# Performance work log

Measured on AMD Instinct MI355X. Metric: run time of the kernel, lower is better.

Reference implementation:

```python
import jax, jax.numpy as jnp
import numpy as np

VOCAB_SIZE = 256
CODEC_VOCAB = 1024  # 2 ** codec_bits
D = 1024
NHEAD = 16
FF = 4096
L = 6
ENROLLED = 225  # enrolled_codec_sec(3) * codec_rate(75)
B, TT, TA = 4, 128, 512


def sinusoidal_pe(T, d):
    pos = np.arange(T, dtype=np.float32)[:, None]
    div = np.exp(np.arange(0, d, 2, dtype=np.float32) * (-np.log(10000.0) / d))
    pe = np.zeros((T, d), dtype=np.float32)
    pe[:, 0::2] = np.sin(pos * div)
    pe[:, 1::2] = np.cos(pos * div)
    return jnp.asarray(pe)


def layernorm(x, w, b, eps=1e-5):
    mu = x.mean(-1, keepdims=True)
    var = ((x - mu) ** 2).mean(-1, keepdims=True)
    return (x - mu) * jax.lax.rsqrt(var + eps) * w + b


def mha(q_in, kv_in, in_w, in_b, out_w, out_b, mask=None):
    # q_in: [B,Tq,D], kv_in: [B,Tk,D]; mask True == blocked (torch attn_mask convention)
    d = q_in.shape[-1]
    h, hd = NHEAD, d // NHEAD
    wq, wk, wv = in_w[:d], in_w[d:2 * d], in_w[2 * d:]
    bq, bk, bv = in_b[:d], in_b[d:2 * d], in_b[2 * d:]
    Bq, Tq, _ = q_in.shape
    Tk = kv_in.shape[1]
    q = (q_in @ wq.T + bq).reshape(Bq, Tq, h, hd)
    k = (kv_in @ wk.T + bk).reshape(Bq, Tk, h, hd)
    v = (kv_in @ wv.T + bv).reshape(Bq, Tk, h, hd)
    scores = jnp.einsum('bqhd,bkhd->bhqk', q, k) / jnp.sqrt(jnp.float32(hd))
    if mask is not None:
        scores = jnp.where(mask, -jnp.inf, scores)
    attn = jax.nn.softmax(scores, axis=-1)
    o = jnp.einsum('bhqk,bkhd->bqhd', attn, v).reshape(Bq, Tq, d)
    return o @ out_w.T + out_b


def pack(te, ae, ee, tl, al):
    # Ragged concat [text[:tl]; audio[:al]; enrolled] padded to static max_len.
    Tt, Ta, Te = te.shape[0], ae.shape[0], ee.shape[0]
    pos = jnp.arange(Tt + Ta + Te)
    t = te[jnp.clip(pos, 0, Tt - 1)]
    a = ae[jnp.clip(pos - tl, 0, Ta - 1)]
    e = ee[jnp.clip(pos - tl - al, 0, Te - 1)]
    x = jnp.where((pos < tl)[:, None], t,
        jnp.where((pos < tl + al)[:, None], a,
        jnp.where((pos < tl + al + Te)[:, None], e, jnp.zeros_like(t))))
    return x


def setup_inputs():
    key = jax.random.key(0)
    ks = iter(jax.random.split(key, 64))

    def n(shape, s=0.02):
        return jax.random.normal(next(ks), shape, dtype=jnp.float32) * s

    text = jax.random.randint(next(ks), (B, TT), 0, VOCAB_SIZE)
    audio = jax.random.randint(next(ks), (B, TA), 0, CODEC_VOCAB)
    enrolled_audio = jax.random.randint(next(ks), (B, ENROLLED), 0, CODEC_VOCAB)
    # force sample 0 to full length so max_len is static (= TT+TA+ENROLLED)
    text_len_batch = jax.random.randint(next(ks), (B,), TT // 2, TT + 1).at[0].set(TT)
    audio_len_batch = jax.random.randint(next(ks), (B,), TA // 2, TA + 1).at[0].set(TA)
    return dict(
        text=text, audio=audio, enrolled_audio=enrolled_audio,
        text_len_batch=text_len_batch, audio_len_batch=audio_len_batch,
        text_emb=n((VOCAB_SIZE, D)), audio_emb=n((CODEC_VOCAB, D)),
        sa_in_w=n((L, 3 * D, D)), sa_in_b=jnp.zeros((L, 3 * D), jnp.float32),
        sa_out_w=n((L, D, D)), sa_out_b=jnp.zeros((L, D), jnp.float32),
        ca_in_w=n((L, 3 * D, D)), ca_in_b=jnp.zeros((L, 3 * D), jnp.float32),
        ca_out_w=n((L, D, D)), ca_out_b=jnp.zeros((L, D), jnp.float32),
        ff1_w=n((L, FF, D)), ff1_b=jnp.zeros((L, FF), jnp.float32),
        ff2_w=n((L, D, FF)), ff2_b=jnp.zeros((L, D), jnp.float32),
        ln1_w=jnp.ones((L, D), jnp.float32), ln1_b=jnp.zeros((L, D), jnp.float32),
        ln2_w=jnp.ones((L, D), jnp.float32), ln2_b=jnp.zeros((L, D), jnp.float32),
        ln3_w=jnp.ones((L, D), jnp.float32), ln3_b=jnp.zeros((L, D), jnp.float32),
        out_w=n((CODEC_VOCAB, D)), out_b=jnp.zeros((CODEC_VOCAB,), jnp.float32))


def reference(text, audio, enrolled_audio, text_len_batch, audio_len_batch,
              text_emb, audio_emb, sa_in_w, sa_in_b, sa_out_w, sa_out_b,
              ca_in_w, ca_in_b, ca_out_w, ca_out_b, ff1_w, ff1_b, ff2_w, ff2_b,
              ln1_w, ln1_b, ln2_w, ln2_b, ln3_w, ln3_b, out_w, out_b):
    # per-segment sinusoidal PE (positions reset at the start of each segment)
    te = text_emb[text] + sinusoidal_pe(text.shape[1], D)
    ae = audio_emb[audio] + sinusoidal_pe(audio.shape[1], D)
    ee = audio_emb[enrolled_audio] + sinusoidal_pe(enrolled_audio.shape[1], D)
    embed = jax.vmap(pack)(te, ae, ee, text_len_batch, audio_len_batch)  # [B, max_len, D]
    max_len = embed.shape[1]
    prefix = text.shape[1] + audio.shape[1]  # == max(tl+al) by construction
    mask = jnp.triu(jnp.ones((max_len, max_len), bool), 1).at[:, :prefix].set(False)
    mem = embed  # TransformerDecoder memory == embed
    x = embed
    for l in range(L):  # post-norm decoder layers (torch default norm_first=False)
        x = layernorm(x + mha(x, x, sa_in_w[l], sa_in_b[l], sa_out_w[l], sa_out_b[l], mask), ln1_w[l], ln1_b[l])
        x = layernorm(x + mha(x, mem, ca_in_w[l], ca_in_b[l], ca_out_w[l], ca_out_b[l]), ln2_w[l], ln2_b[l])
        h = jax.nn.relu(x @ ff1_w[l].T + ff1_b[l]) @ ff2_w[l].T + ff2_b[l]
        x = layernorm(x + h, ln3_w[l], ln3_b[l])
    return x @ out_w.T + out_b  # [B, max_len, CODEC_VOCAB]
```

## Files before the change

### kernel.cpp

```cpp
#include <hip/hip_runtime.h>
#include <hip/hip_bf16.h>

#define B_      4
#define TT_     128
#define TA_     512
#define TE_     225
#define T_      865
#define D_      1024
#define H_      16
#define FF_     4096
#define L_      6
#define PREFIX_ 640
#define M_TOK   (B_ * T_)
#define M_PAD   3584

typedef __attribute__((ext_vector_type(8))) short          s16x8;
typedef __attribute__((ext_vector_type(4))) float          f32x4;
typedef __attribute__((ext_vector_type(8))) unsigned short u16x8;

typedef __attribute__((address_space(1))) const void gv_t;
typedef __attribute__((address_space(3))) void       lv_t;

__device__ __forceinline__ float bf2f(unsigned short u) {
  union { unsigned int i; float f; } c; c.i = ((unsigned int)u) << 16; return c.f;
}
__device__ __forceinline__ unsigned short f2bf(float f) {
  union { __hip_bfloat16 h; unsigned short u; } c; c.h = __float2bfloat16(f); return c.u;
}

__global__ __launch_bounds__(256) void embed_kernel(
    const int* __restrict__ text, const int* __restrict__ audio,
    const int* __restrict__ enrolled, const int* __restrict__ tl_b,
    const int* __restrict__ al_b, const float* __restrict__ text_emb,
    const float* __restrict__ audio_emb,
    float* __restrict__ xf, unsigned short* __restrict__ xb,
    unsigned short* __restrict__ memb, unsigned short* __restrict__ attnb) {
  int row = blockIdx.x;
  int d0 = threadIdx.x * 4;
  size_t off = (size_t)row * D_ + d0;
  if (row >= M_TOK) {
    *(unsigned long long*)&xb[off]    = 0ull;
    *(unsigned long long*)&memb[off]  = 0ull;
    *(unsigned long long*)&attnb[off] = 0ull;
    return;
  }
  int b = row / T_, pos = row - b * T_;
  int tl = tl_b[b], al = al_b[b];
  const float* emb = nullptr;
  int p = 0;
  if (pos < tl) {
    emb = text_emb + (size_t)text[b * TT_ + pos] * D_;
    p = pos;
  } else if (pos < tl + al) {
    emb = audio_emb + (size_t)audio[b * TA_ + (pos - tl)] * D_;
    p = pos - tl;
  } else if (pos < tl + al + TE_) {
    emb = audio_emb + (size_t)enrolled[b * TE_ + (pos - tl - al)] * D_;
    p = pos - tl - al;
  }
  float4 v;
  float* pv = (float*)&v;
  if (emb) {
    const float c = -9.2103403719761836f / (float)D_;
    #pragma unroll
    for (int e = 0; e < 4; ++e) {
      int d = d0 + e;
      int i = d >> 1;
      float freq = expf(c * (float)(2 * i));
      float arg = (float)p * freq;
      float pe = (d & 1) ? cosf(arg) : sinf(arg);
      pv[e] = emb[d] + pe;
    }
  } else {
    v = make_float4(0.f, 0.f, 0.f, 0.f);
  }
  *(float4*)&xf[off] = v;
  unsigned long long pk = (unsigned long long)f2bf(pv[0])
      | ((unsigned long long)f2bf(pv[1]) << 16)
      | ((unsigned long long)f2bf(pv[2]) << 32)
      | ((unsigned long long)f2bf(pv[3]) << 48);
  *(unsigned long long*)&xb[off]   = pk;
  *(unsigned long long*)&memb[off] = pk;
}

__global__ __launch_bounds__(256) void cvt_kernel(
    const float* __restrict__ in, unsigned short* __restrict__ out, int n8) {
  int i = blockIdx.x * 256 + threadIdx.x;
  if (i >= n8) return;
  const float4* pp = (const float4*)in + (size_t)i * 2;
  float4 a = pp[0], bq = pp[1];
  u16x8 o;
  o[0] = f2bf(a.x);  o[1] = f2bf(a.y);  o[2] = f2bf(a.z);  o[3] = f2bf(a.w);
  o[4] = f2bf(bq.x); o[5] = f2bf(bq.y); o[6] = f2bf(bq.z); o[7] = f2bf(bq.w);
  *(u16x8*)(out + (size_t)i * 8) = o;
}

__global__ __launch_bounds__(256) void cvt_layer_kernel(
    const float* __restrict__ s0, const float* __restrict__ s1,
    const float* __restrict__ s2, const float* __restrict__ s3,
    const float* __restrict__ s4, const float* __restrict__ s5,
    unsigned short* __restrict__ dst) {
  size_t e = ((size_t)blockIdx.x * 256 + threadIdx.x) * 8;
  if (e >= 16777216u) return;
  const float* src; size_t off;
  if      (e <  3145728u) { src = s0; off = e; }
  else if (e <  4194304u) { src = s1; off = e -  3145728u; }
  else if (e <  7340032u) { src = s2; off = e -  4194304u; }
  else if (e <  8388608u) { src = s3; off = e -  7340032u; }
  else if (e < 12582912u) { src = s4; off = e -  8388608u; }
  else                    { src = s5; off = e - 12582912u; }
  const float4* pp = (const float4*)(src + off);
  float4 a = pp[0], bq = pp[1];
  u16x8 o;
  o[0] = f2bf(a.x);  o[1] = f2bf(a.y);  o[2] = f2bf(a.z);  o[3] = f2bf(a.w);
  o[4] = f2bf(bq.x); o[5] = f2bf(bq.y); o[6] = f2bf(bq.z); o[7] = f2bf(bq.w);
  *(u16x8*)(dst + e) = o;
}

template <int BM, int BN, int ACT, int OBF>
__global__ __launch_bounds__(256) void gemm_bf16(
    const unsigned short* __restrict__ A, int lda,
    const unsigned short* __restrict__ W, int ldw,
    const float* __restrict__ bias,
    float* __restrict__ Cf, unsigned short* __restrict__ Cb, int ldc,
    int Mw, int K) {
  constexpr int WROWS = BM / 2, WCOLS = BN / 2;
  constexpr int WM = WROWS / 16, WN = WCOLS / 16;
  constexpr int ACH = BM / 64, BCH = BN / 64;
  __shared__ unsigned short lgA[2][BM * 32];
  __shared__ unsigned short lgB[2][BN * 32];
  int tid = threadIdx.x, lane = tid & 63, wid = tid >> 6;

  int gx = gridDim.x;
  int nwg = gx * gridDim.y;
  int orig = blockIdx.y * gx + blockIdx.x;
  int q = nwg >> 3, r = nwg & 7;
  int xcd = orig & 7, loc = orig >> 3;
  int wg = (xcd < r ? xcd * (q + 1) : r * (q + 1) + (xcd - r) * q) + loc;
  int m0 = (wg / gx) * BM, n0 = (wg % gx) * BN;

  int wr = wid >> 1, wc = wid & 1;
  int lrow = lane >> 2, lk = (lane & 3) * 8;

  const unsigned short* gAp[ACH];
  const unsigned short* gBp[BCH];
  unsigned aoff[ACH], boff[BCH];
  #pragma unroll
  for (int c = 0; c < ACH; ++c) {
    int row0 = wid * (16 * ACH) + 16 * c;
    gAp[c] = A + (size_t)(m0 + row0 + lrow) * lda + lk;
    aoff[c] = row0 * 32;
  }
  #pragma unroll
  for (int c = 0; c < BCH; ++c) {
    int row0 = wid * (16 * BCH) + 16 * c;
    gBp[c] = W + (size_t)(n0 + row0 + lrow) * ldw + lk;
    boff[c] = row0 * 32;
  }

  f32x4 acc[WM][WN];
  #pragma unroll
  for (int i = 0; i < WM; ++i)
    #pragma unroll
    for (int j = 0; j < WN; ++j) acc[i][j] = (f32x4)0.f;

  int frow = lane & 15, fk = (lane >> 4) * 8;

  #pragma unroll
  for (int c = 0; c < ACH; ++c)
    __builtin_amdgcn_global_load_lds((gv_t*)gAp[c], (lv_t*)&lgA[0][aoff[c]], 16, 0, 0);
  #pragma unroll
  for (int c = 0; c < BCH; ++c)
    __builtin_amdgcn_global_load_lds((gv_t*)gBp[c], (lv_t*)&lgB[0][boff[c]], 16, 0, 0);
  __syncthreads();

  int nt = K / 32;
  for (int t = 0; t < nt; ++t) {
    int cur = t & 1;
    if (t + 1 < nt) {
      int k0 = (t + 1) * 32;
      #pragma unroll
      for (int c = 0; c < ACH; ++c)
        __builtin_amdgcn_global_load_lds((gv_t*)(gAp[c] + k0),
                                         (lv_t*)&lgA[cur ^ 1][aoff[c]], 16, 0, 0);
      #pragma unroll
      for (int c = 0; c < BCH; ++c)
        __builtin_amdgcn_global_load_lds((gv_t*)(gBp[c] + k0),
                                         (lv_t*)&lgB[cur ^ 1][boff[c]], 16, 0, 0);
    }
    s16x8 af[WM], bfr[WN];
    #pragma unroll
    for (int i = 0; i < WM; ++i)
      af[i] = *(const s16x8*)&lgA[cur][(wr * WROWS + i * 16 + frow) * 32 + fk];
    #pragma unroll
    for (int j = 0; j < WN; ++j)
      bfr[j] = *(const s16x8*)&lgB[cur][(wc * WCOLS + j * 16 + frow) * 32 + fk];
    __builtin_amdgcn_s_setprio(1);
    #pragma unroll
    for (int i = 0; i < WM; ++i)
      #pragma unroll
      for (int j = 0; j < WN; ++j)
        acc[i][j] = __builtin_amdgcn_mfma_f32_16x16x32_bf16(af[i], bfr[j], acc[i][j], 0, 0, 0);
    __builtin_amdgcn_s_setprio(0);
    __syncthreads();
  }

  float bv[WN];
  #pragma unroll
  for (int j = 0; j < WN; ++j) bv[j] = bias[n0 + wc * WCOLS + j * 16 + (lane & 15)];
  int rbase = m0 + wr * WROWS + (lane >> 4) * 4;
  int cbase = n0 + wc * WCOLS + (lane & 15);
  #pragma unroll
  for (int i = 0; i < WM; ++i)
    #pragma unroll
    for (int rr = 0; rr < 4; ++rr) {
      int m = rbase + i * 16 + rr;
      if (m < Mw) {
        #pragma unroll
        for (int j = 0; j < WN; ++j) {
          float v = acc[i][j][rr] + bv[j];
          if (ACT) v = fmaxf(v, 0.f);
          if (OBF) Cb[(size_t)m * ldc + cbase + j * 16] = f2bf(v);
          else     Cf[(size_t)m * ldc + cbase + j * 16] = v;
        }
      }
    }
}

template <bool MASKED>
__global__ __launch_bounds__(256) void attn_mfma(
    const unsigned short* __restrict__ qkv,
    unsigned short* __restrict__ out) {
  __shared__ unsigned short KsL[64 * 64];
  __shared__ unsigned short VtL[64 * 72];
  __shared__ unsigned short PsL[4][16 * 64];
  int tid = threadIdx.x;
  int lane = tid & 63, wid = tid >> 6;
  int b = blockIdx.y >> 4, h = blockIdx.y & 15;
  int q0 = blockIdx.x * 64;
  int r16 = lane & 15, g4 = lane >> 4;

  int qrow = q0 + wid * 16 + r16;
  if (qrow >= T_) qrow = T_ - 1;
  const unsigned short* qbase =
      qkv + (size_t)(b * T_ + qrow) * 3072 + h * 64 + g4 * 8;
  s16x8 qf0 = *(const s16x8*)qbase;
  s16x8 qf1 = *(const s16x8*)(qbase + 32);

  float m_[4], l_[4];
  f32x4 o_[4];
  #pragma unroll
  for (int rg = 0; rg < 4; ++rg) { m_[rg] = -INFINITY; l_[rg] = 0.f; }
  #pragma unroll
  for (int dj = 0; dj < 4; ++dj) o_[dj] = (f32x4)0.f;

  const int nt = MASKED ? max(10, (int)blockIdx.x + 1) : 14;

  for (int t = 0; t < nt; ++t) {
    int k0 = t * 64;
    __syncthreads();

    #pragma unroll
    for (int c = 0; c < 2; ++c) {
      int row = wid * 16 + c * 8 + (lane >> 3);
      int kr = k0 + row; if (kr >= T_) kr = T_ - 1;
      int grp = (lane & 7) ^ (row & 7);
      const unsigned short* src =
          qkv + (size_t)(b * T_ + kr) * 3072 + 1024 + h * 64 + grp * 8;
      __builtin_amdgcn_global_load_lds((gv_t*)src,
          (lv_t*)&KsL[(wid * 16 + c * 8) * 64], 16, 0, 0);
    }
    {
      int vkr = k0 + lane; if (vkr >= T_) vkr = T_ - 1;
      const unsigned short* vsrc =
          qkv + (size_t)(b * T_ + vkr) * 3072 + 2048 + h * 64 + wid * 16;
      u16x8 v0 = *(const u16x8*)vsrc;
      u16x8 v1 = *(const u16x8*)(vsrc + 8);
      #pragma unroll
      for (int jj = 0; jj < 8; ++jj) {
        VtL[(wid * 16 + jj) * 72 + lane]     = v0[jj];
        VtL[(wid * 16 + 8 + jj) * 72 + lane] = v1[jj];
      }
    }
    __syncthreads();

    f32x4 sj[4];
    #pragma unroll
    for (int j = 0; j < 4; ++j) sj[j] = (f32x4)0.f;
    __builtin_amdgcn_s_setprio(1);
    #pragma unroll
    for (int j = 0; j < 4; ++j) {
      int krow = j * 16 + r16;
      s16x8 kf0 = *(const s16x8*)&KsL[krow * 64 + ((g4 ^ (krow & 7)) * 8)];
      s16x8 kf1 = *(const s16x8*)&KsL[krow * 64 + (((4 + g4) ^ (krow & 7)) * 8)];
      sj[j] = __builtin_amdgcn_mfma_f32_16x16x32_bf16(qf0, kf0, sj[j], 0, 0, 0);
      sj[j] = __builtin_amdgcn_mfma_f32_16x16x32_bf16(qf1, kf1, sj[j], 0, 0, 0);
    }
    __builtin_amdgcn_s_setprio(0);

    float alpha_[4];
    #pragma unroll
    for (int rg = 0; rg < 4; ++rg) {
      int qa = q0 + wid * 16 + g4 * 4 + rg;
      float pm = -INFINITY;
      #pragma unroll
      for (int j = 0; j < 4; ++j) {
        int kg = k0 + j * 16 + r16;
        float sv = sj[j][rg] * 0.125f;
        bool bad = (kg >= T_) || (MASKED && kg > qa && kg >= PREFIX_);
        sv = bad ? -INFINITY : sv;
        sj[j][rg] = sv;
        pm = fmaxf(pm, sv);
      }
      pm = fmaxf(pm, __shfl_xor(pm, 1));
      pm = fmaxf(pm, __shfl_xor(pm, 2));
      pm = fmaxf(pm, __shfl_xor(pm, 4));
      pm = fmaxf(pm, __shfl_xor(pm, 8));
      float mn = fmaxf(m_[rg], pm);
      float al = __expf(m_[rg] - mn);
      m_[rg] = mn;
      alpha_[rg] = al;
      int prow = g4 * 4 + rg;
      float ps = 0.f;
      #pragma unroll
      for (int j = 0; j < 4; ++j) {
        float pv = __expf(sj[j][rg] - mn);
        ps += pv;
        PsL[wid][prow * 64 + (((j * 2 + (r16 >> 3)) ^ (prow & 7)) * 8) + (r16 & 7)]
            = f2bf(pv);
      }
      ps += __shfl_xor(ps, 1);
      ps += __shfl_xor(ps, 2);
      ps += __shfl_xor(ps, 4);
      ps += __shfl_xor(ps, 8);
      l_[rg] = l_[rg] * al + ps;
    }
    #pragma unroll
    for (int dj = 0; dj < 4; ++dj)
      #pragma unroll
      for (int rg = 0; rg < 4; ++rg) o_[dj][rg] *= alpha_[rg];

    __builtin_amdgcn_s_setprio(1);
    #pragma unroll
    for (int kk = 0; kk < 2; ++kk) {
      s16x8 pf = *(const s16x8*)
          &PsL[wid][r16 * 64 + (((kk * 4 + g4) ^ (r16 & 7)) * 8)];
      #pragma unroll
      for (int dj = 0; dj < 4; ++dj) {
        s16x8 vf = *(const s16x8*)
            &VtL[(dj * 16 + r16) * 72 + kk * 32 + g4 * 8];
        o_[dj] = __builtin_amdgcn_mfma_f32_16x16x32_bf16(pf, vf, o_[dj], 0, 0, 0);
      }
    }
    __builtin_amdgcn_s_setprio(0);
  }

  #pragma unroll
  for (int rg = 0; rg < 4; ++rg) {
    int qa = q0 + wid * 16 + g4 * 4 + rg;
    if (qa < T_) {
      float inv = 1.f / l_[rg];
      unsigned short* ob = out + (size_t)(b * T_ + qa) * D_ + h * 64;
      #pragma unroll
      for (int dj = 0; dj < 4; ++dj)
        ob[dj * 16 + r16] = f2bf(o_[dj][rg] * inv);
    }
  }
}

__global__ __launch_bounds__(256) void ln_res_kernel(
    float* __restrict__ x, const float* __restrict__ r,
    const float* __restrict__ w, const float* __restrict__ b,
    unsigned short* __restrict__ xb) {
  __shared__ float red[4];
  int row = blockIdx.x, tid = threadIdx.x;
  size_t off = (size_t)row * D_ + tid * 4;
  float4 xv = *(float4*)&x[off];
  float4 rv = *(const float4*)&r[off];
  float v0 = xv.x + rv.x, v1 = xv.y + rv.y, v2 = xv.z + rv.z, v3 = xv.w + rv.w;

  float s = v0 + v1 + v2 + v3;
  #pragma unroll
  for (int o = 1; o < 64; o <<= 1) s += __shfl_xor(s, o);
  if ((tid & 63) == 0) red[tid >> 6] = s;
  __syncthreads();
  float mu = (red[0] + red[1] + red[2] + red[3]) * (1.f / 1024.f);
  __syncthreads();

  float d0 = v0 - mu, d1 = v1 - mu, d2 = v2 - mu, d3 = v3 - mu;
  float ss = d0 * d0 + d1 * d1 + d2 * d2 + d3 * d3;
  #pragma unroll
  for (int o = 1; o < 64; o <<= 1) ss += __shfl_xor(ss, o);
  if ((tid & 63) == 0) red[tid >> 6] = ss;
  __syncthreads();
  float var = (red[0] + red[1] + red[2] + red[3]) * (1.f / 1024.f);
  float rs = rsqrtf(var + 1e-5f);

  float4 wv = *(const float4*)&w[tid * 4];
  float4 bv = *(const float4*)&b[tid * 4];
  float o0 = d0 * rs * wv.x + bv.x, o1 = d1 * rs * wv.y + bv.y;
  float o2 = d2 * rs * wv.z + bv.z, o3 = d3 * rs * wv.w + bv.w;
  *(float4*)&x[off] = make_float4(o0, o1, o2, o3);
  unsigned long long pk = (unsigned long long)f2bf(o0)
      | ((unsigned long long)f2bf(o1) << 16)
      | ((unsigned long long)f2bf(o2) << 32)
      | ((unsigned long long)f2bf(o3) << 48);
  *(unsigned long long*)&xb[off] = pk;
}

extern "C" void kernel_launch(void* const* d_in, const int* in_sizes, int n_in,
                              void* d_out, int out_size, void* d_ws, size_t ws_size,
                              hipStream_t stream) {
  const int* text       = (const int*)d_in[0];
  const int* audio      = (const int*)d_in[1];
  const int* enrolled   = (const int*)d_in[2];
  const int* tl_b       = (const int*)d_in[3];
  const int* al_b       = (const int*)d_in[4];
  const float* text_emb = (const float*)d_in[5];
  const float* audio_emb= (const float*)d_in[6];
  const float* sa_in_w  = (const float*)d_in[7];
  const float* sa_in_b  = (const float*)d_in[8];
  const float* sa_out_w = (const float*)d_in[9];
  const float* sa_out_b = (const float*)d_in[10];
  const float* ca_in_w  = (const float*)d_in[11];
  const float* ca_in_b  = (const float*)d_in[12];
  const float* ca_out_w = (const float*)d_in[13];
  const float* ca_out_b = (const float*)d_in[14];
  const float* ff1_w    = (const float*)d_in[15];
  const float* ff1_b    = (const float*)d_in[16];
  const float* ff2_w    = (const float*)d_in[17];
  const float* ff2_b    = (const float*)d_in[18];
  const float* ln1_w    = (const float*)d_in[19];
  const float* ln1_b    = (const float*)d_in[20];
  const float* ln2_w    = (const float*)d_in[21];
  const float* ln2_b    = (const float*)d_in[22];
  const float* ln3_w    = (const float*)d_in[23];
  const float* ln3_b    = (const float*)d_in[24];
  const float* out_w    = (const float*)d_in[25];
  const float* out_b    = (const float*)d_in[26];

  char* p = (char*)d_ws;
  float* xf = (float*)p;            p += (size_t)M_PAD * D_ * 4;
  float* tmp = (float*)p;           p += (size_t)M_PAD * D_ * 4;
  unsigned short* xb = (unsigned short*)p;    p += (size_t)M_PAD * D_ * 2;
  unsigned short* memb = (unsigned short*)p;  p += (size_t)M_PAD * D_ * 2;
  unsigned short* qkv = (unsigned short*)p;   p += (size_t)M_PAD * FF_ * 2;
  unsigned short* attnb = (unsigned short*)p; p += (size_t)M_PAD * D_ * 2;
  unsigned short* wbuf = (unsigned short*)p;  p += (size_t)16777216 * 2;
  unsigned short* outwb = (unsigned short*)p; p += (size_t)1048576 * 2;

  unsigned short* w_sa_qkv = wbuf;
  unsigned short* w_sa_o   = wbuf + 3145728;
  unsigned short* w_ca_qkv = wbuf + 4194304;
  unsigned short* w_ca_o   = wbuf + 7340032;
  unsigned short* w_ff1    = wbuf + 8388608;
  unsigned short* w_ff2    = wbuf + 12582912;

  embed_kernel<<<M_PAD, 256, 0, stream>>>(text, audio, enrolled, tl_b, al_b,
                                          text_emb, audio_emb, xf, xb, memb, attnb);
  cvt_kernel<<<512, 256, 0, stream>>>(out_w, outwb, 131072);

  for (int l = 0; l < L_; ++l) {
    const float* sa_in_w_l  = sa_in_w  + (size_t)l * 3 * D_ * D_;
    const float* sa_in_b_l  = sa_in_b  + (size_t)l * 3 * D_;
    const float* sa_out_w_l = sa_out_w + (size_t)l * D_ * D_;
    const float* sa_out_b_l = sa_out_b + (size_t)l * D_;
    const float* ca_in_w_l  = ca_in_w  + (size_t)l * 3 * D_ * D_;
    const float* ca_in_b_l  = ca_in_b  + (size_t)l * 3 * D_;
    const float* ca_out_w_l = ca_out_w + (size_t)l * D_ * D_;
    const float* ca_out_b_l = ca_out_b + (size_t)l * D_;
    const float* ff1_w_l    = ff1_w    + (size_t)l * FF_ * D_;
    const float* ff1_b_l    = ff1_b    + (size_t)l * FF_;
    const float* ff2_w_l    = ff2_w    + (size_t)l * D_ * FF_;
    const float* ff2_b_l    = ff2_b    + (size_t)l * D_;

    cvt_layer_kernel<<<8192, 256, 0, stream>>>(sa_in_w_l, sa_out_w_l, ca_in_w_l,
                                               ca_out_w_l, ff1_w_l, ff2_w_l, wbuf);

    gemm_bf16<128, 128, 0, 1><<<dim3(3 * D_ / 128, M_PAD / 128), 256, 0, stream>>>(
        xb, D_, w_sa_qkv, D_, sa_in_b_l, nullptr, qkv, 3 * D_, M_PAD, D_);
    attn_mfma<true><<<dim3(14, B_ * H_), 256, 0, stream>>>(qkv, attnb);
    gemm_bf16<64, 64, 0, 0><<<dim3(D_ / 64, M_PAD / 64), 256, 0, stream>>>(
        attnb, D_, w_sa_o, D_, sa_out_b_l, tmp, nullptr, D_, M_PAD, D_);
    ln_res_kernel<<<M_TOK, 256, 0, stream>>>(xf, tmp, ln1_w + l * D_, ln1_b + l * D_, xb);

    gemm_bf16<64, 64, 0, 1><<<dim3(D_ / 64, M_PAD / 64), 256, 0, stream>>>(
        xb, D_, w_ca_qkv, D_, ca_in_b_l, nullptr, qkv, 3 * D_, M_PAD, D_);
    gemm_bf16<64, 64, 0, 1><<<dim3(2 * D_ / 64, M_PAD / 64), 256, 0, stream>>>(
        memb, D_, w_ca_qkv + (size_t)D_ * D_, D_, ca_in_b_l + D_,
        nullptr, qkv + D_, 3 * D_, M_PAD, D_);
    attn_mfma<false><<<dim3(14, B_ * H_), 256, 0, stream>>>(qkv, attnb);
    gemm_bf16<64, 64, 0, 0><<<dim3(D_ / 64, M_PAD / 64), 256, 0, stream>>>(
        attnb, D_, w_ca_o, D_, ca_out_b_l, tmp, nullptr, D_, M_PAD, D_);
    ln_res_kernel<<<M_TOK, 256, 0, stream>>>(xf, tmp, ln2_w + l * D_, ln2_b + l * D_, xb);

    gemm_bf16<128, 128, 1, 1><<<dim3(FF_ / 128, M_PAD / 128), 256, 0, stream>>>(
        xb, D_, w_ff1, D_, ff1_b_l, nullptr, qkv, FF_, M_PAD, D_);
    gemm_bf16<64, 64, 0, 0><<<dim3(D_ / 64, M_PAD / 64), 256, 0, stream>>>(
        qkv, FF_, w_ff2, FF_, ff2_b_l, tmp, nullptr, D_, M_PAD, FF_);
    ln_res_kernel<<<M_TOK, 256, 0, stream>>>(xf, tmp, ln3_w + l * D_, ln3_b + l * D_, xb);
  }

  gemm_bf16<64, 64, 0, 0><<<dim3(D_ / 64, M_PAD / 64), 256, 0, stream>>>(
      xb, D_, outwb, D_, out_b, (float*)d_out, nullptr, D_, M_TOK, D_);
}
```

Before: 2.288 ms.

## Triple-buffer GEMM with swizzled LDS and batch cross-attention KV projections across layers

Replaces the double-buffered GEMM with a three-stage pipeline. It uses explicit vmcnt waits, a single barrier per iteration, an XOR-swizzled LDS layout to avoid bank conflicts, and BK=64 for the 64x64 tiles. Because cross-attention K/V depend only on the fixed memory, the K/V weights for all six layers are converted once and projected in one large GEMM up front. This removes six smaller per-layer GEMMs and gives better tile utilization. The cost is a large extra workspace buffer, with a fallback path used when the workspace is too small.

New measurement: 2.216 ms. 3.1% less time.

```diff
diff --git a/kernel.cpp b/kernel.cpp
--- a/kernel.cpp
+++ b/kernel.cpp
@@ -13,6 +13,7 @@
 #define PREFIX_ 640
 #define M_TOK   (B_ * T_)
 #define M_PAD   3584
+#define NKV     (L_ * 2 * D_)
 
 typedef __attribute__((ext_vector_type(8))) short          s16x8;
 typedef __attribute__((ext_vector_type(4))) float          f32x4;
@@ -26,6 +27,9 @@
 }
 __device__ __forceinline__ unsigned short f2bf(float f) {
   union { __hip_bfloat16 h; unsigned short u; } c; c.h = __float2bfloat16(f); return c.u;
+}
+template <int N> __device__ __forceinline__ void vmwait() {
+  asm volatile("s_waitcnt vmcnt(%0)" :: "n"(N) : "memory");
 }
 
 __global__ __launch_bounds__(256) void embed_kernel(
@@ -117,8 +121,31 @@
   *(u16x8*)(dst + e) = o;
 }
 
-template <int BM, int BN, int ACT, int OBF>
-__global__ __launch_bounds__(256) void gemm_bf16(
+__global__ __launch_bounds__(256) void cvt_ckv_w(
+    const float* __restrict__ ca_in_w, unsigned short* __restrict__ wckv) {
+  int rr = blockIdx.x;
+  int l = rr / (2 * D_), w = rr % (2 * D_);
+  const float* src = ca_in_w + (size_t)l * 3 * D_ * D_ + (size_t)(D_ + w) * D_;
+  unsigned short* dst = wckv + (size_t)rr * D_;
+  int c = threadIdx.x * 4;
+  float4 v4 = *(const float4*)(src + c);
+  unsigned long long pk = (unsigned long long)f2bf(v4.x)
+      | ((unsigned long long)f2bf(v4.y) << 16)
+      | ((unsigned long long)f2bf(v4.z) << 32)
+      | ((unsigned long long)f2bf(v4.w) << 48);
+  *(unsigned long long*)&dst[c] = pk;
+}
+
+__global__ __launch_bounds__(256) void cvt_ckv_b(
+    const float* __restrict__ ca_in_b, float* __restrict__ cbias) {
+  int rr = blockIdx.x * 256 + threadIdx.x;
+  if (rr >= NKV) return;
+  int l = rr / (2 * D_), w = rr % (2 * D_);
+  cbias[rr] = ca_in_b[(size_t)l * 3 * D_ + D_ + w];
+}
+
+template <int BM, int BN, int BK, int ACT, int OBF>
+__global__ __launch_bounds__(256) void gemm_p2(
     const unsigned short* __restrict__ A, int lda,
     const unsigned short* __restrict__ W, int ldw,
     const float* __restrict__ bias,
@@ -126,11 +153,16 @@
     int Mw, int K) {
   constexpr int WROWS = BM / 2, WCOLS = BN / 2;
   constexpr int WM = WROWS / 16, WN = WCOLS / 16;
-  constexpr int ACH = BM / 64, BCH = BN / 64;
-  __shared__ unsigned short lgA[2][BM * 32];
-  __shared__ unsigned short lgB[2][BN * 32];
+  constexpr int LPR = BK / 8;
+  constexpr int RPI = 64 / LPR;
+  constexpr int ACH = (BM / 4) / RPI;
+  constexpr int BCH = (BN / 4) / RPI;
+  constexpr int ABUF = BM * BK, BBUF = BN * BK;
+  constexpr int KSUB = BK / 32;
+  constexpr int LW = ACH + BCH;
+  __shared__ unsigned short lds[3 * (ABUF + BBUF)];
+
   int tid = threadIdx.x, lane = tid & 63, wid = tid >> 6;
-
   int gx = gridDim.x;
   int nwg = gx * gridDim.y;
   int orig = blockIdx.y * gx + blockIdx.x;
@@ -140,22 +172,23 @@
   int m0 = (wg / gx) * BM, n0 = (wg % gx) * BN;
 
   int wr = wid >> 1, wc = wid & 1;
-  int lrow = lane >> 2, lk = (lane & 3) * 8;
-
-  const unsigned short* gAp[ACH];
-  const unsigned short* gBp[BCH];
-  unsigned aoff[ACH], boff[BCH];
+  int lrow = lane / LPR, lgrp = lane % LPR;
+  int skey = (BK == 32) ? ((lrow >> 1) & 3) : (lrow & 7);
+  int lk = (lgrp ^ skey) * 8;
+
+  const unsigned short* gAp[ACH]; unsigned aoff[ACH];
+  const unsigned short* gBp[BCH]; unsigned boff[BCH];
   #pragma unroll
   for (int c = 0; c < ACH; ++c) {
-    int row0 = wid * (16 * ACH) + 16 * c;
+    int row0 = wid * (BM / 4) + c * RPI;
     gAp[c] = A + (size_t)(m0 + row0 + lrow) * lda + lk;
-    aoff[c] = row0 * 32;
+    aoff[c] = row0 * BK;
   }
   #pragma unroll
   for (int c = 0; c < BCH; ++c) {
-    int row0 = wid * (16 * BCH) + 16 * c;
+    int row0 = wid * (BN / 4) + c * RPI;
     gBp[c] = W + (size_t)(n0 + row0 + lrow) * ldw + lk;
-    boff[c] = row0 * 32;
+    boff[c] = row0 * BK;
   }
 
   f32x4 acc[WM][WN];
@@ -164,45 +197,53 @@
     #pragma unroll
     for (int j = 0; j < WN; ++j) acc[i][j] = (f32x4)0.f;
 
-  int frow = lane & 15, fk = (lane >> 4) * 8;
-
-  #pragma unroll
-  for (int c = 0; c < ACH; ++c)
-    __builtin_amdgcn_global_load_lds((gv_t*)gAp[c], (lv_t*)&lgA[0][aoff[c]], 16, 0, 0);
-  #pragma unroll
-  for (int c = 0; c < BCH; ++c)
-    __builtin_amdgcn_global_load_lds((gv_t*)gBp[c], (lv_t*)&lgB[0][boff[c]], 16, 0, 0);
-  __syncthreads();
-
-  int nt = K / 32;
+  int frow = lane & 15, g4 = lane >> 4;
+
+  auto STAGE = [&](int bi, int t) {
+    int k0 = t * BK;
+    #pragma unroll
+    for (int c = 0; c < ACH; ++c)
+      __builtin_amdgcn_global_load_lds((gv_t*)(gAp[c] + k0),
+          (lv_t*)&lds[bi * ABUF + aoff[c]], 16, 0, 0);
+    #pragma unroll
+    for (int c = 0; c < BCH; ++c)
+      __builtin_amdgcn_global_load_lds((gv_t*)(gBp[c] + k0),
+          (lv_t*)&lds[3 * ABUF + bi * BBUF + boff[c]], 16, 0, 0);
+  };
+
+  STAGE(0, 0);
+  STAGE(1, 1);
+  int nt = K / BK;
+  int cur = 0;
   for (int t = 0; t < nt; ++t) {
-    int cur = t & 1;
-    if (t + 1 < nt) {
-      int k0 = (t + 1) * 32;
-      #pragma unroll
-      for (int c = 0; c < ACH; ++c)
-        __builtin_amdgcn_global_load_lds((gv_t*)(gAp[c] + k0),
-                                         (lv_t*)&lgA[cur ^ 1][aoff[c]], 16, 0, 0);
-      #pragma unroll
-      for (int c = 0; c < BCH; ++c)
-        __builtin_amdgcn_global_load_lds((gv_t*)(gBp[c] + k0),
-                                         (lv_t*)&lgB[cur ^ 1][boff[c]], 16, 0, 0);
-    }
-    s16x8 af[WM], bfr[WN];
-    #pragma unroll
-    for (int i = 0; i < WM; ++i)
-      af[i] = *(const s16x8*)&lgA[cur][(wr * WROWS + i * 16 + frow) * 32 + fk];
-    #pragma unroll
-    for (int j = 0; j < WN; ++j)
-      bfr[j] = *(const s16x8*)&lgB[cur][(wc * WCOLS + j * 16 + frow) * 32 + fk];
-    __builtin_amdgcn_s_setprio(1);
-    #pragma unroll
-    for (int i = 0; i < WM; ++i)
+    if (t + 1 < nt) vmwait<LW>(); else vmwait<0>();
+    __builtin_amdgcn_s_barrier();
+    if (t + 2 < nt) {
+      int stb = cur + 2; if (stb >= 3) stb -= 3;
+      STAGE(stb, t + 2);
+    }
+    const unsigned short* Ab = &lds[cur * ABUF];
+    const unsigned short* Bb = &lds[3 * ABUF + cur * BBUF];
+    #pragma unroll
+    for (int kk = 0; kk < KSUB; ++kk) {
+      int rk = (BK == 32) ? ((g4 ^ ((frow >> 1) & 3)) * 8)
+                          : (((kk * 4 + g4) ^ (frow & 7)) * 8);
+      s16x8 af[WM], bfr[WN];
+      #pragma unroll
+      for (int i = 0; i < WM; ++i)
+        af[i] = *(const s16x8*)&Ab[(wr * WROWS + i * 16 + frow) * BK + rk];
       #pragma unroll
       for (int j = 0; j < WN; ++j)
-        acc[i][j] = __builtin_amdgcn_mfma_f32_16x16x32_bf16(af[i], bfr[j], acc[i][j], 0, 0, 0);
-    __builtin_amdgcn_s_setprio(0);
-    __syncthreads();
+        bfr[j] = *(const s16x8*)&Bb[(wc * WCOLS + j * 16 + frow) * BK + rk];
+      __builtin_amdgcn_s_setprio(1);
+      #pragma unroll
+      for (int i = 0; i < WM; ++i)
+        #pragma unroll
+        for (int j = 0; j < WN; ++j)
+          acc[i][j] = __builtin_amdgcn_mfma_f32_16x16x32_bf16(af[i], bfr[j], acc[i][j], 0, 0, 0);
+      __builtin_amdgcn_s_setprio(0);
+    }
+    cur = (cur == 2) ? 0 : cur + 1;
   }
 
   float bv[WN];
@@ -229,7 +270,9 @@
 
 template <bool MASKED>
 __global__ __launch_bounds__(256) void attn_mfma(
-    const unsigned short* __restrict__ qkv,
+    const unsigned short* __restrict__ qp, int qld,
+    const unsigned short* __restrict__ kp,
+    const unsigned short* __restrict__ vp, int kvld,
     unsigned short* __restrict__ out) {
   __shared__ unsigned short KsL[64 * 64];
   __shared__ unsigned short VtL[64 * 72];
@@ -243,7 +286,7 @@
   int qrow = q0 + wid * 16 + r16;
   if (qrow >= T_) qrow = T_ - 1;
   const unsigned short* qbase =
-      qkv + (size_t)(b * T_ + qrow) * 3072 + h * 64 + g4 * 8;
+      qp + (size_t)(b * T_ + qrow) * qld + h * 64 + g4 * 8;
   s16x8 qf0 = *(const s16x8*)qbase;
   s16x8 qf1 = *(const s16x8*)(qbase + 32);
 
@@ -266,14 +309,14 @@
       int kr = k0 + row; if (kr >= T_) kr = T_ - 1;
       int grp = (lane & 7) ^ (row & 7);
       const unsigned short* src =
-          qkv + (size_t)(b * T_ + kr) * 3072 + 1024 + h * 64 + grp * 8;
+          kp + (size_t)(b * T_ + kr) * kvld + h * 64 + grp * 8;
       __builtin_amdgcn_global_load_lds((gv_t*)src,
           (lv_t*)&KsL[(wid * 16 + c * 8) * 64], 16, 0, 0);
     }
     {
       int vkr = k0 + lane; if (vkr >= T_) vkr = T_ - 1;
       const unsigned short* vsrc =
-          qkv + (size_t)(b * T_ + vkr) * 3072 + 2048 + h * 64 + wid * 16;
+          vp + (size_t)(b * T_ + vkr) * kvld + h * 64 + wid * 16;
       u16x8 v0 = *(const u16x8*)vsrc;
       u16x8 v1 = *(const u16x8*)(vsrc + 8);
       #pragma unroll
@@ -448,6 +491,10 @@
   unsigned short* attnb = (unsigned short*)p; p += (size_t)M_PAD * D_ * 2;
   unsigned short* wbuf = (unsigned short*)p;  p += (size_t)16777216 * 2;
   unsigned short* outwb = (unsigned short*)p; p += (size_t)1048576 * 2;
+  unsigned short* ckv  = (unsigned short*)p;  p += (size_t)M_PAD * NKV * 2;
+  unsigned short* wckv = (unsigned short*)p;  p += (size_t)NKV * D_ * 2;
+  float* cbias = (float*)p;                   p += (size_t)NKV * 4;
+  bool fused = ((size_t)(p - (char*)d_ws)) <= ws_size;
 
   unsigned short* w_sa_qkv = wbuf;
   unsigned short* w_sa_o   = wbuf + 3145728;
@@ -459,6 +506,13 @@
   embed_kernel<<<M_PAD, 256, 0, stream>>>(text, audio, enrolled, tl_b, al_b,
                                           text_emb, audio_emb, xf, xb, memb, attnb);
   cvt_kernel<<<512, 256, 0, stream>>>(out_w, outwb, 131072);
+
+  if (fused) {
+    cvt_ckv_w<<<NKV, 256, 0, stream>>>(ca_in_w, wckv);
+    cvt_ckv_b<<<NKV / 256, 256, 0, stream>>>(ca_in_b, cbias);
+    gemm_p2<128, 128, 32, 0, 1><<<dim3(NKV / 128, M_PAD / 128), 256, 0, stream>>>(
+        memb, D_, wckv, D_, cbias, nullptr, ckv, NKV, M_PAD, D_);
+  }
 
   for (int l = 0; l < L_; ++l) {
     const float* sa_in_w_l  = sa_in_w  + (size_t)l * 3 * D_ * D_;
@@ -477,30 +531,38 @@
     cvt_layer_kernel<<<8192, 256, 0, stream>>>(sa_in_w_l, sa_out_w_l, ca_in_w_l,
                                                ca_out_w_l, ff1_w_l, ff2_w_l, wbuf);
 
-    gemm_bf16<128, 128, 0, 1><<<dim3(3 * D_ / 128, M_PAD / 128), 256, 0, stream>>>(
+    gemm_p2<128, 128, 32, 0, 1><<<dim3(3 * D_ / 128, M_PAD / 128), 256, 0, stream>>>(
         xb, D_, w_sa_qkv, D_, sa_in_b_l, nullptr, qkv, 3 * D_, M_PAD, D_);
-    attn_mfma<true><<<dim3(14, B_ * H_), 256, 0, stream>>>(qkv, attnb);
-    gemm_bf16<64, 64, 0, 0><<<dim3(D_ / 64, M_PAD / 64), 256, 0, stream>>>(
+    attn_mfma<true><<<dim3(14, B_ * H_), 256, 0, stream>>>(
+        qkv, 3 * D_, qkv + D_, qkv + 2 * D_, 3 * D_, attnb);
+    gemm_p2<64, 64, 64, 0, 0><<<dim3(D_ / 64, M_PAD / 64), 256, 0, stream>>>(
         attnb, D_, w_sa_o, D_, sa_out_b_l, tmp, nullptr, D_, M_PAD, D_);
     ln_res_kernel<<<M_TOK, 256, 0, stream>>>(xf, tmp, ln1_w + l * D_, ln1_b + l * D_, xb);
 
-    gemm_bf16<64, 64, 0, 1><<<dim3(D_ / 64, M_PAD / 64), 256, 0, stream>>>(
+    gemm_p2<64, 64, 64, 0, 1><<<dim3(D_ / 64, M_PAD / 64), 256, 0, stream>>>(
         xb, D_, w_ca_qkv, D_, ca_in_b_l, nullptr, qkv, 3 * D_, M_PAD, D_);
-    gemm_bf16<64, 64, 0, 1><<<dim3(2 * D_ / 64, M_PAD / 64), 256, 0, stream>>>(
-        memb, D_, w_ca_qkv + (size_t)D_ * D_, D_, ca_in_b_l + D_,
-        nullptr, qkv + D_, 3 * D_, M_PAD, D_);
-    attn_mfma<false><<<dim3(14, B_ * H_), 256, 0, stream>>>(qkv, attnb);
-    gemm_bf16<64, 64, 0, 0><<<dim3(D_ / 64, M_PAD / 64), 256, 0, stream>>>(
+    if (fused) {
+      attn_mfma<false><<<dim3(14, B_ * H_), 256, 0, stream>>>(
+          qkv, 3 * D_, ckv + (size_t)l * 2 * D_, ckv + (size_t)l * 2 * D_ + D_,
+          NKV, attnb);
+    } else {
+      gemm_p2<64, 64, 64, 0, 1><<<dim3(2 * D_ / 64, M_PAD / 64), 256, 0, stream>>>(
+          memb, D_, w_ca_qkv + (size_t)D_ * D_, D_, ca_in_b_l + D_,
+          nullptr, qkv + D_, 3 * D_, M_PAD, D_);
+      attn_mfma<false><<<dim3(14, B_ * H_), 256, 0, stream>>>(
+          qkv, 3 * D_, qkv + D_, qkv + 2 * D_, 3 * D_, attnb);
+    }
+    gemm_p2<64, 64, 64, 0, 0><<<dim3(D_ / 64, M_PAD / 64), 256, 0, stream>>>(
         attnb, D_, w_ca_o, D_, ca_out_b_l, tmp, nullptr, D_, M_PAD, D_);
     ln_res_kernel<<<M_TOK, 256, 0, stream>>>(xf, tmp, ln2_w + l * D_, ln2_b + l * D_, xb);
 
-    gemm_bf16<128, 128, 1, 1><<<dim3(FF_ / 128, M_PAD / 128), 256, 0, stream>>>(
+    gemm_p2<128, 128, 32, 1, 1><<<dim3(FF_ / 128, M_PAD / 128), 256, 0, stream>>>(
         xb, D_, w_ff1, D_, ff1_b_l, nullptr, qkv, FF_, M_PAD, D_);
-    gemm_bf16<64, 64, 0, 0><<<dim3(D_ / 64, M_PAD / 64), 256, 0, stream>>>(
+    gemm_p2<64, 64, 64, 0, 0><<<dim3(D_ / 64, M_PAD / 64), 256, 0, stream>>>(
         qkv, FF_, w_ff2, FF_, ff2_b_l, tmp, nullptr, D_, M_PAD, FF_);
     ln_res_kernel<<<M_TOK, 256, 0, stream>>>(xf, tmp, ln3_w + l * D_, ln3_b + l * D_, xb);
   }
 
-  gemm_bf16<64, 64, 0, 0><<<dim3(D_ / 64, M_PAD / 64), 256, 0, stream>>>(
+  gemm_p2<64, 64, 64, 0, 0><<<dim3(D_ / 64, M_PAD / 64), 256, 0, stream>>>(
       xb, D_, outwb, D_, out_b, (float*)d_out, nullptr, D_, M_TOK, D_);
 }
```
